# Performance work log

Hardware: AMD Instinct MI355X
Metric: run time of the kernel (lower is better)

Reference implementation:

```python
import jax, jax.numpy as jnp
import numpy as np

B, N, D_OBJ, D_Q, D_FUSED, D_BOX, D_ATT = 64, 36, 2048, 2048, 2048, 4, 512


def setup_inputs() -> dict:
    key = jax.random.key(0)
    ks = jax.random.split(key, 12)
    s = lambda d: 1.0 / np.sqrt(d)
    return {
        "question_embedding": jax.random.normal(ks[0], (B * N, D_Q), jnp.float32),
        "object_features_list": jax.random.normal(ks[1], (B, N, D_OBJ), jnp.float32),
        "bounding_boxes": jax.random.uniform(ks[2], (B, N, D_BOX), jnp.float32),
        "Wq": jax.random.normal(ks[3], (D_Q, D_FUSED), jnp.float32) * s(D_Q),
        "Wo": jax.random.normal(ks[4], (D_OBJ, D_FUSED), jnp.float32) * s(D_OBJ),
        "Wfa": jax.random.normal(ks[5], (D_FUSED, D_FUSED), jnp.float32) * s(D_FUSED),
        "Wfb": jax.random.normal(ks[6], (D_FUSED, D_FUSED), jnp.float32) * s(D_FUSED),
        "Wba": jax.random.normal(ks[7], (D_BOX, D_FUSED), jnp.float32) * s(D_BOX),
        "Wbb": jax.random.normal(ks[8], (D_BOX, D_FUSED), jnp.float32) * s(D_BOX),
        "W0": jax.random.normal(ks[9], (D_FUSED, D_ATT), jnp.float32) * s(D_FUSED),
        "b0": jnp.zeros((D_ATT,), jnp.float32),
        "W1": jax.random.normal(ks[10], (D_ATT, 1), jnp.float32) * s(D_ATT),
        "b1": jnp.zeros((1,), jnp.float32),
        "batch_size": B,
        "num_obj": N,
    }


def reference(question_embedding, object_features_list, bounding_boxes,
              Wq, Wo, Wfa, Wfb, Wba, Wbb, W0, b0, W1, b1,
              batch_size, num_obj):
    # fuse_object_features_with_questions: MLB fusion of question and objects
    obj_flat = object_features_list.reshape(batch_size * num_obj, -1)  # [BN, D]
    fused = (question_embedding @ Wq) * (obj_flat @ Wo)                # [BN, Df]
    fused = fused.reshape(batch_size, num_obj, -1)                     # [B, N, Df]

    # pairwise: project once, broadcast-multiply instead of materializing
    # expanded [B*N*N, D] operands (same math as expand+view+fusion).
    ra = fused @ Wfa                 # [B, N, Df]
    rb = fused @ Wfb                 # [B, N, Df]
    ba = bounding_boxes @ Wba        # [B, N, Df]
    bb = bounding_boxes @ Wbb        # [B, N, Df]
    # relations[b, i, j, :] = fusion_fused(f_i, f_j) + fusion_box(box_i, box_j)
    relations = ra[:, :, None, :] * rb[:, None, :, :] + ba[:, :, None, :] * bb[:, None, :, :]  # [B,N,N,Df]

    # compute_relation_attention: linear-tanh-linear, softmax over dim=2
    h = jnp.tanh(relations @ W0 + b0)          # [B, N, N, D_att]
    scores = h @ W1 + b1                       # [B, N, N, 1]
    att = jax.nn.softmax(scores, axis=2)[..., 0]  # [B, N, N]
    e_hat = jnp.sum(relations * att[..., None], axis=2)  # [B, N, Df]

    pairwise_res = fused + e_hat
    return object_features_list + pairwise_res
```

## Files before the change

kernel.cpp:

```cpp
#include <hip/hip_runtime.h>
#include <hip/hip_bf16.h>
#include <math.h>

constexpr int kB    = 64;
constexpr int kN    = 36;
constexpr int kBN   = kB * kN;
constexpr int kD    = 2048;
constexpr int kDatt = 512;
constexpr int kPairs = kN * kN;

using bf16x8 = __attribute__((ext_vector_type(8))) short;
using f32x4  = __attribute__((ext_vector_type(4))) float;

typedef unsigned int u32;
typedef __attribute__((address_space(3))) u32 lds_u32;
typedef const __attribute__((address_space(1))) u32 glb_u32;

__device__ inline unsigned short f2bf(float f) {
    union { float f; unsigned u; } v; v.f = f;
    unsigned r = v.u + 0x7FFFu + ((v.u >> 16) & 1u);
    return (unsigned short)(r >> 16);
}

__global__ __launch_bounds__(256)
void kcvt(const float* __restrict__ x, unsigned short* __restrict__ y, int n4)
{
    int i = blockIdx.x * 256 + threadIdx.x;
    if (i < n4) {
        float4 v = ((const float4*)x)[i];
        ushort4 o = {f2bf(v.x), f2bf(v.y), f2bf(v.z), f2bf(v.w)};
        ((ushort4*)y)[i] = o;
    }
}

__global__ __launch_bounds__(256)
void ktrp(const float* __restrict__ W, unsigned short* __restrict__ WT, int nt)
{
    __shared__ float T[64][65];
    const int k0 = blockIdx.x * 64;
    const int n0 = blockIdx.y * 64;
    const int c = threadIdx.x & 63, r0 = threadIdx.x >> 6;
    #pragma unroll
    for (int rr = 0; rr < 64; rr += 4)
        T[r0 + rr][c] = W[(size_t)(k0 + r0 + rr) * nt + n0 + c];
    __syncthreads();
    #pragma unroll
    for (int rr = 0; rr < 64; rr += 4)
        WT[(size_t)(n0 + r0 + rr) * kD + k0 + c] = f2bf(T[c][r0 + rr]);
}

__global__ __launch_bounds__(64)
void krepack_w0(const unsigned short* __restrict__ W0T, unsigned short* __restrict__ W0s)
{
    const int kb    = blockIdx.x;
    const int chunk = blockIdx.y;
    const int g     = threadIdx.x;
    const int row = chunk * 16 + (g & 7) + ((g >> 5) << 3);
    const int cg8 = ((g >> 3) & 3) * 8;
    const uint4 v = *(const uint4*)&W0T[(size_t)row * kD + kb * 32 + cg8];
    *(uint4*)&W0s[(size_t)kb * 16384 + chunk * 512 + g * 8] = v;
}

__global__ __launch_bounds__(256)
void k3_box_proj(const float* __restrict__ box, const float* __restrict__ Wba,
                 const float* __restrict__ Wbb,
                 float* __restrict__ ba, float* __restrict__ bb)
{
    const int r = blockIdx.y;
    const int c = blockIdx.x * 256 + threadIdx.x;
    const float x0 = box[r * 4 + 0], x1 = box[r * 4 + 1];
    const float x2 = box[r * 4 + 2], x3 = box[r * 4 + 3];
    float va = x0 * Wba[c] + x1 * Wba[kD + c] + x2 * Wba[2 * kD + c] + x3 * Wba[3 * kD + c];
    float vb = x0 * Wbb[c] + x1 * Wbb[kD + c] + x2 * Wbb[2 * kD + c] + x3 * Wbb[3 * kD + c];
    ba[(size_t)r * kD + c] = va;
    bb[(size_t)r * kD + c] = vb;
}

__device__ inline void stage128(const unsigned short* __restrict__ g,
                                int grow0, int k0,
                                unsigned short* lds, int w, int lane)
{
    const int sr = lane >> 2, sc = (lane & 3) * 8;
    #pragma unroll
    for (int t = 0; t < 2; ++t) {
        int r = w * 32 + t * 16;
        const unsigned short* gp = g + (size_t)(grow0 + r + sr) * kD + k0 + sc;
        __builtin_amdgcn_global_load_lds((glb_u32*)gp, (lds_u32*)(lds + r * 32), 16, 0, 0);
    }
}
__device__ inline void stage64(const unsigned short* __restrict__ g,
                               int grow0, int k0,
                               unsigned short* lds, int w, int lane)
{
    const int sr = lane >> 2, sc = (lane & 3) * 8;
    int r = w * 16;
    const unsigned short* gp = g + (size_t)(grow0 + r + sr) * kD + k0 + sc;
    __builtin_amdgcn_global_load_lds((glb_u32*)gp, (lds_u32*)(lds + r * 32), 16, 0, 0);
}

__global__ __launch_bounds__(256, 2)
void k1_dual_mfma(const unsigned short* __restrict__ Qb,
                  const unsigned short* __restrict__ WqT,
                  const unsigned short* __restrict__ Ob,
                  const unsigned short* __restrict__ WoT,
                  unsigned short* __restrict__ fusedb)
{
    __shared__ __align__(16) unsigned short As1[128][32];
    __shared__ __align__(16) unsigned short As2[128][32];
    __shared__ __align__(16) unsigned short Bs1[64][32];
    __shared__ __align__(16) unsigned short Bs2[64][32];

    const int tid = threadIdx.x;
    const int lane = tid & 63;
    const int w = tid >> 6;
    const int wm = w >> 1, wn = w & 1;
    const int row0 = blockIdx.y * 128;
    const int col0 = blockIdx.x * 64;

    f32x4 acc1[4][2], acc2[4][2];
    #pragma unroll
    for (int mt = 0; mt < 4; ++mt)
        #pragma unroll
        for (int nt = 0; nt < 2; ++nt) { acc1[mt][nt] = (f32x4)(0.f); acc2[mt][nt] = (f32x4)(0.f); }

    const int fr = lane & 15, ko = (lane >> 4) * 8;

    for (int k0 = 0; k0 < kD; k0 += 32) {
        stage128(Qb,  row0, k0, &As1[0][0], w, lane);
        stage128(Ob,  row0, k0, &As2[0][0], w, lane);
        stage64 (WqT, col0, k0, &Bs1[0][0], w, lane);
        stage64 (WoT, col0, k0, &Bs2[0][0], w, lane);
        __syncthreads();

        bf16x8 a1[4], a2[4];
        #pragma unroll
        for (int mt = 0; mt < 4; ++mt) {
            a1[mt] = *(bf16x8*)&As1[wm * 64 + mt * 16 + fr][ko];
            a2[mt] = *(bf16x8*)&As2[wm * 64 + mt * 16 + fr][ko];
        }
        #pragma unroll
        for (int nt = 0; nt < 2; ++nt) {
            bf16x8 b1 = *(bf16x8*)&Bs1[wn * 32 + nt * 16 + fr][ko];
            bf16x8 b2 = *(bf16x8*)&Bs2[wn * 32 + nt * 16 + fr][ko];
            #pragma unroll
            for (int mt = 0; mt < 4; ++mt) {
                acc1[mt][nt] = __builtin_amdgcn_mfma_f32_16x16x32_bf16(a1[mt], b1, acc1[mt][nt], 0, 0, 0);
                acc2[mt][nt] = __builtin_amdgcn_mfma_f32_16x16x32_bf16(a2[mt], b2, acc2[mt][nt], 0, 0, 0);
            }
        }
        __syncthreads();
    }

    const int fq = lane >> 4;
    #pragma unroll
    for (int mt = 0; mt < 4; ++mt)
        #pragma unroll
        for (int nt = 0; nt < 2; ++nt) {
            int row = row0 + wm * 64 + mt * 16 + fq * 4;
            int col = col0 + wn * 32 + nt * 16 + fr;
            #pragma unroll
            for (int reg = 0; reg < 4; ++reg) {
                float v = acc1[mt][nt][reg] * acc2[mt][nt][reg];
                fusedb[(size_t)(row + reg) * kD + col] = f2bf(v);
            }
        }
}

__global__ __launch_bounds__(256, 2)
void k2_dual_mfma(const unsigned short* __restrict__ Fb,
                  const unsigned short* __restrict__ WfaT,
                  const unsigned short* __restrict__ WfbT,
                  float* __restrict__ ra, float* __restrict__ rb)
{
    __shared__ __align__(16) unsigned short As [128][32];
    __shared__ __align__(16) unsigned short Bs1[64][32];
    __shared__ __align__(16) unsigned short Bs2[64][32];

    const int tid = threadIdx.x;
    const int lane = tid & 63;
    const int w = tid >> 6;
    const int wm = w >> 1, wn = w & 1;
    const int row0 = blockIdx.y * 128;
    const int col0 = blockIdx.x * 64;

    f32x4 acc1[4][2], acc2[4][2];
    #pragma unroll
    for (int mt = 0; mt < 4; ++mt)
        #pragma unroll
        for (int nt = 0; nt < 2; ++nt) { acc1[mt][nt] = (f32x4)(0.f); acc2[mt][nt] = (f32x4)(0.f); }

    const int fr = lane & 15, ko = (lane >> 4) * 8;

    for (int k0 = 0; k0 < kD; k0 += 32) {
        stage128(Fb,   row0, k0, &As [0][0], w, lane);
        stage64 (WfaT, col0, k0, &Bs1[0][0], w, lane);
        stage64 (WfbT, col0, k0, &Bs2[0][0], w, lane);
        __syncthreads();

        bf16x8 a[4];
        #pragma unroll
        for (int mt = 0; mt < 4; ++mt)
            a[mt] = *(bf16x8*)&As[wm * 64 + mt * 16 + fr][ko];
        #pragma unroll
        for (int nt = 0; nt < 2; ++nt) {
            bf16x8 b1 = *(bf16x8*)&Bs1[wn * 32 + nt * 16 + fr][ko];
            bf16x8 b2 = *(bf16x8*)&Bs2[wn * 32 + nt * 16 + fr][ko];
            #pragma unroll
            for (int mt = 0; mt < 4; ++mt) {
                acc1[mt][nt] = __builtin_amdgcn_mfma_f32_16x16x32_bf16(a[mt], b1, acc1[mt][nt], 0, 0, 0);
                acc2[mt][nt] = __builtin_amdgcn_mfma_f32_16x16x32_bf16(a[mt], b2, acc2[mt][nt], 0, 0, 0);
            }
        }
        __syncthreads();
    }

    const int fq = lane >> 4;
    #pragma unroll
    for (int mt = 0; mt < 4; ++mt)
        #pragma unroll
        for (int nt = 0; nt < 2; ++nt) {
            int row = row0 + wm * 64 + mt * 16 + fq * 4;
            int col = col0 + wn * 32 + nt * 16 + fr;
            #pragma unroll
            for (int reg = 0; reg < 4; ++reg) {
                size_t o = (size_t)(row + reg) * kD + col;
                ra[o] = acc1[mt][nt][reg];
                rb[o] = acc2[mt][nt][reg];
            }
        }
}

__global__ __launch_bounds__(1024)
void k4_scores_mfma(const float* __restrict__ ra, const float* __restrict__ rb,
                    const float* __restrict__ ba, const float* __restrict__ bb,
                    const unsigned short* __restrict__ W0s,
                    const float* __restrict__ b0, const float* __restrict__ W1,
                    float* __restrict__ scores)
{
    __shared__ __align__(16) unsigned short Bs[2][512 * 32];
    __shared__ __align__(16) unsigned short RelS[2][128][40];
    __shared__ __align__(16) float4 Stg4[2][714];
    __shared__ float scoreS[128];

    const int tid  = threadIdx.x;
    const int lane = tid & 63;
    const int w    = tid >> 6;
    const int wm   = w >> 3;
    const int wn   = w & 7;

    const int work = (blockIdx.x & 7) * 88 + (blockIdx.x >> 3);
    const int b    = work / 11;
    const int tile = work - b * 11;
    const int p0   = tile * 128;
    const int i0   = p0 / kN;

    const float* raB = ra + (size_t)b * kN * kD;
    const float* rbB = rb + (size_t)b * kN * kD;
    const float* baB = ba + (size_t)b * kN * kD;
    const float* bbB = bb + (size_t)b * kN * kD;

    const bool hasStage = (tid < 672);
    const float* sptr;
    int sdst;
    {
        int s = hasStage ? tid : 671;
        int row = s >> 4, t4 = s & 15;
        int arr = t4 >> 3, q = t4 & 7;
        int grow; const float* base;
        if (row < 6) {
            int il = (row < 5) ? row : 4;
            grow = i0 + il; if (grow > kN - 1) grow = kN - 1;
            base = arr ? baB : raB;
        } else {
            grow = row - 6;
            base = arr ? bbB : rbB;
        }
        sptr = base + (size_t)grow * kD + q * 4;
        sdst = row * 17 + t4;
    }

    int rowA, cgA, ilA, jA;
    {
        rowA = tid >> 3; cgA = tid & 7;
        int p = p0 + rowA; if (p >= kPairs) p = kPairs - 1;
        int i = p / kN;
        jA  = p - i * kN;
        ilA = i - i0;
    }

    const int fr = lane & 15, fq = lane >> 4;
    const int bco = ((fr & 7) << 3) + ((fr >> 3) << 8) + (fq << 6);

    f32x4 acc[4][4];
    #pragma unroll
    for (int mt = 0; mt < 4; ++mt)
        #pragma unroll
        for (int nt = 0; nt < 4; ++nt)
            acc[mt][nt] = (f32x4)(0.f);

    if (tid < 128) scoreS[tid] = 0.f;

    float4 sreg0;

    #define ISSUE_B(k0_, buf_)                                                   \
        _Pragma("unroll")                                                        \
        for (int t = 0; t < 2; ++t) {                                            \
            int chunk = w * 2 + t;                                               \
            const unsigned short* gp = W0s + (size_t)((k0_) >> 5) * 16384        \
                                       + chunk * 512 + lane * 8;                 \
            __builtin_amdgcn_global_load_lds((glb_u32*)gp,                       \
                (lds_u32*)&Bs[buf_][chunk * 512], 16, 0, 0);                     \
        }

    #define STAGE_LOAD(k0_) {                                                    \
            if (hasStage) sreg0 = *(const float4*)(sptr + (k0_));                \
        }

    #define STAGE_WRITE(buf_) {                                                  \
            if (hasStage) Stg4[buf_][sdst] = sreg0;                              \
        }

    #define REL_GEN(buf_) {                                                      \
            float4 va = Stg4[buf_][ilA * 17 + cgA];                              \
            float4 vb = Stg4[buf_][ilA * 17 + 8 + cgA];                          \
            float4 vr = Stg4[buf_][(6 + jA) * 17 + cgA];                         \
            float4 vq = Stg4[buf_][(6 + jA) * 17 + 8 + cgA];                     \
            ushort4 o;                                                           \
            o.x = f2bf(va.x * vr.x + vb.x * vq.x);                               \
            o.y = f2bf(va.y * vr.y + vb.y * vq.y);                               \
            o.z = f2bf(va.z * vr.z + vb.z * vq.z);                               \
            o.w = f2bf(va.w * vr.w + vb.w * vq.w);                               \
            *(ushort4*)&RelS[buf_][rowA][cgA * 4] = o;                           \
        }

    STAGE_LOAD(0)
    STAGE_WRITE(0)
    STAGE_LOAD(32)
    __syncthreads();
    REL_GEN(0)
    STAGE_WRITE(1)
    ISSUE_B(0, 0)

    for (int k = 0; k < 64; ++k) {
        const int cur = k & 1, nxt = cur ^ 1;
        __syncthreads();
        if (k < 62) STAGE_LOAD((k + 2) * 32)
        if (k < 63) ISSUE_B((k + 1) * 32, nxt)
        bf16x8 af[4];
        #pragma unroll
        for (int mt = 0; mt < 4; ++mt)
            af[mt] = *(bf16x8*)&RelS[cur][wm * 64 + mt * 16 + fr][fq * 8];
        #pragma unroll
        for (int nt = 0; nt < 4; ++nt) {
            bf16x8 bfv = *(bf16x8*)&Bs[cur][wn * 2048 + nt * 512 + bco];
            #pragma unroll
            for (int mt = 0; mt < 4; ++mt)
                acc[mt][nt] = __builtin_amdgcn_mfma_f32_16x16x32_bf16(af[mt], bfv, acc[mt][nt], 0, 0, 0);
        }
        if (k < 62) STAGE_WRITE(cur)
        if (k < 63) REL_GEN(nxt)
    }

    float b0v[4], w1v[4];
    #pragma unroll
    for (int nt = 0; nt < 4; ++nt) {
        int col = wn * 64 + nt * 16 + fr;
        b0v[nt] = b0[col];
        w1v[nt] = W1[col];
    }
    #pragma unroll
    for (int mt = 0; mt < 4; ++mt) {
        #pragma unroll
        for (int reg = 0; reg < 4; ++reg) {
            float p = 0.f;
            #pragma unroll
            for (int nt = 0; nt < 4; ++nt)
                p += w1v[nt] * tanhf(acc[mt][nt][reg] + b0v[nt]);
            p += __shfl_xor(p, 1, 64);
            p += __shfl_xor(p, 2, 64);
            p += __shfl_xor(p, 4, 64);
            p += __shfl_xor(p, 8, 64);
            if (fr == 0)
                atomicAdd(&scoreS[wm * 64 + mt * 16 + fq * 4 + reg], p);
        }
    }
    __syncthreads();
    if (tid < 128 && p0 + tid < kPairs)
        scores[(size_t)b * kPairs + p0 + tid] = scoreS[tid];
}

__global__ __launch_bounds__(64)
void k5_softmax(const float* __restrict__ scores, float* __restrict__ att)
{
    const int bi = blockIdx.x;
    const int tid = threadIdx.x;
    float s = (tid < kN) ? scores[(size_t)bi * kN + tid] : -1e30f;
    float m = s;
    #pragma unroll
    for (int off = 32; off >= 1; off >>= 1)
        m = fmaxf(m, __shfl_xor(m, off, 64));
    float e = (tid < kN) ? expf(s - m) : 0.f;
    float sum = e;
    #pragma unroll
    for (int off = 32; off >= 1; off >>= 1)
        sum += __shfl_xor(sum, off, 64);
    if (tid < kN) att[(size_t)bi * kN + tid] = e / sum;
}

__global__ __launch_bounds__(256)
void k6_output(const float* __restrict__ obj, const unsigned short* __restrict__ fusedb,
               const float* __restrict__ ra, const float* __restrict__ ba,
               const float* __restrict__ rb, const float* __restrict__ bb,
               const float* __restrict__ att, float* __restrict__ out)
{
    __shared__ float attS[kN];
    const int bi = blockIdx.x;
    const int b = bi / kN;
    const int tid = threadIdx.x;
    if (tid < kN) attS[tid] = att[(size_t)bi * kN + tid];
    __syncthreads();
    for (int d = tid; d < kD; d += 256) {
        float s1 = 0.f, s2 = 0.f;
        #pragma unroll 4
        for (int j = 0; j < kN; ++j) {
            float a = attS[j];
            size_t rrow = (size_t)(b * kN + j) * kD + d;
            s1 = fmaf(a, rb[rrow], s1);
            s2 = fmaf(a, bb[rrow], s2);
        }
        size_t o = (size_t)bi * kD + d;
        float fv = __uint_as_float((u32)fusedb[o] << 16);
        out[o] = obj[o] + fv + ra[o] * s1 + ba[o] * s2;
    }
}

extern "C" void kernel_launch(void* const* d_in, const int* in_sizes, int n_in,
                              void* d_out, int out_size, void* d_ws, size_t ws_size,
                              hipStream_t stream)
{
    const float* q   = (const float*)d_in[0];
    const float* obj = (const float*)d_in[1];
    const float* box = (const float*)d_in[2];
    const float* Wq  = (const float*)d_in[3];
    const float* Wo  = (const float*)d_in[4];
    const float* Wfa = (const float*)d_in[5];
    const float* Wfb = (const float*)d_in[6];
    const float* Wba = (const float*)d_in[7];
    const float* Wbb = (const float*)d_in[8];
    const float* W0  = (const float*)d_in[9];
    const float* b0v = (const float*)d_in[10];
    const float* W1  = (const float*)d_in[11];
    float* out = (float*)d_out;

    const size_t nBD = (size_t)kBN * kD;
    float* ws = (float*)d_ws;
    size_t off = 0;
    float* ra     = ws + off; off += nBD;
    float* rb     = ws + off; off += nBD;
    float* ba     = ws + off; off += nBD;
    float* bb     = ws + off; off += nBD;
    float* scores = ws + off; off += (size_t)kBN * kN;
    float* att    = ws + off; off += (size_t)kBN * kN;

    unsigned short* us = (unsigned short*)(ws + off);
    size_t uoff = 0;
    unsigned short* W0T     = us + uoff; uoff += (size_t)kDatt * kD;
    unsigned short* W0s     = us + uoff; uoff += (size_t)kDatt * kD;
    unsigned short* q_bf    = us + uoff; uoff += nBD;
    unsigned short* obj_bf  = us + uoff; uoff += nBD;
    unsigned short* fusedbf = us + uoff; uoff += nBD;
    unsigned short* WqT     = us + uoff; uoff += (size_t)kD * kD;
    unsigned short* WoT     = us + uoff; uoff += (size_t)kD * kD;
    unsigned short* WfaT = q_bf;
    unsigned short* WfbT = obj_bf;

    const int n4 = (int)(nBD / 4);
    kcvt<<<dim3((n4 + 255) / 256), 256, 0, stream>>>(q,   q_bf,   n4);
    kcvt<<<dim3((n4 + 255) / 256), 256, 0, stream>>>(obj, obj_bf, n4);
    ktrp<<<dim3(32, 32), 256, 0, stream>>>(Wq, WqT, kD);
    ktrp<<<dim3(32, 32), 256, 0, stream>>>(Wo, WoT, kD);
    ktrp<<<dim3(32, 8),  256, 0, stream>>>(W0, W0T, kDatt);
    krepack_w0<<<dim3(kD / 32, kDatt / 16), 64, 0, stream>>>(W0T, W0s);
    k3_box_proj<<<dim3(kD / 256, kBN), 256, 0, stream>>>(box, Wba, Wbb, ba, bb);

    k1_dual_mfma<<<dim3(kD / 64, kBN / 128), 256, 0, stream>>>(q_bf, WqT, obj_bf, WoT, fusedbf);

    ktrp<<<dim3(32, 32), 256, 0, stream>>>(Wfa, WfaT, kD);
    ktrp<<<dim3(32, 32), 256, 0, stream>>>(Wfb, WfbT, kD);

    k2_dual_mfma<<<dim3(kD / 64, kBN / 128), 256, 0, stream>>>(fusedbf, WfaT, WfbT, ra, rb);

    k4_scores_mfma<<<dim3(kB * 11), 1024, 0, stream>>>(ra, rb, ba, bb, W0s, b0v, W1, scores);
    k5_softmax<<<kBN, 64, 0, stream>>>(scores, att);
    k6_output<<<kBN, 256, 0, stream>>>(obj, fusedbf, ra, ba, rb, bb, att, out);
}
```

Baseline: 666.4 us.

## Fold box relation term into precomputed W0 projection as extra K step

```diff
diff --git a/kernel.cpp b/kernel.cpp
--- a/kernel.cpp
+++ b/kernel.cpp
@@ -59,6 +59,39 @@
     const int cg8 = ((g >> 3) & 3) * 8;
     const uint4 v = *(const uint4*)&W0T[(size_t)row * kD + kb * 32 + cg8];
     *(uint4*)&W0s[(size_t)kb * 16384 + chunk * 512 + g * 8] = v;
+}
+
+__global__ __launch_bounds__(128)
+void kgbox(const float* __restrict__ Wba, const float* __restrict__ Wbb,
+           const float* __restrict__ W0, float* __restrict__ G)
+{
+    const int uv = blockIdx.x;
+    const int u = uv >> 2, v = uv & 3;
+    const int c = blockIdx.y * 128 + threadIdx.x;
+    float acc = 0.f;
+    for (int k = 0; k < kD; k += 4) {
+        #pragma unroll
+        for (int t = 0; t < 4; ++t)
+            acc = fmaf(Wba[u * kD + k + t] * Wbb[v * kD + k + t],
+                       W0[(size_t)(k + t) * kDatt + c], acc);
+    }
+    G[(size_t)uv * kDatt + c] = acc;
+}
+
+__global__ __launch_bounds__(64)
+void krepack_g(const float* __restrict__ G, unsigned short* __restrict__ W0s)
+{
+    const int chunk = blockIdx.x;
+    const int g     = threadIdx.x;
+    const int col = chunk * 16 + (g & 7) + ((g >> 5) << 3);
+    const int kg  = (g >> 3) & 3;
+    unsigned short o[8];
+    #pragma unroll
+    for (int e = 0; e < 8; ++e) {
+        int kl = kg * 8 + e;
+        o[e] = (kl < 16) ? f2bf(G[(size_t)kl * kDatt + col]) : (unsigned short)0;
+    }
+    *(uint4*)&W0s[(size_t)64 * 16384 + chunk * 512 + g * 8] = *(uint4*)o;
 }
 
 __global__ __launch_bounds__(256)
@@ -232,14 +265,14 @@
 
 __global__ __launch_bounds__(1024)
 void k4_scores_mfma(const float* __restrict__ ra, const float* __restrict__ rb,
-                    const float* __restrict__ ba, const float* __restrict__ bb,
+                    const float* __restrict__ box,
                     const unsigned short* __restrict__ W0s,
                     const float* __restrict__ b0, const float* __restrict__ W1,
                     float* __restrict__ scores)
 {
     __shared__ __align__(16) unsigned short Bs[2][512 * 32];
     __shared__ __align__(16) unsigned short RelS[2][128][40];
-    __shared__ __align__(16) float4 Stg4[2][714];
+    __shared__ __align__(16) float4 Stg4[2][378];
     __shared__ float scoreS[128];
 
     const int tid  = threadIdx.x;
@@ -254,38 +287,36 @@
     const int p0   = tile * 128;
     const int i0   = p0 / kN;
 
-    const float* raB = ra + (size_t)b * kN * kD;
-    const float* rbB = rb + (size_t)b * kN * kD;
-    const float* baB = ba + (size_t)b * kN * kD;
-    const float* bbB = bb + (size_t)b * kN * kD;
-
-    const bool hasStage = (tid < 672);
+    const float* raB  = ra  + (size_t)b * kN * kD;
+    const float* rbB  = rb  + (size_t)b * kN * kD;
+    const float* boxB = box + (size_t)b * kN * 4;
+
+    const bool hasStage = (tid < 336);
     const float* sptr;
     int sdst;
     {
-        int s = hasStage ? tid : 671;
-        int row = s >> 4, t4 = s & 15;
-        int arr = t4 >> 3, q = t4 & 7;
+        int s = hasStage ? tid : 335;
+        int row = s >> 3, q = s & 7;
         int grow; const float* base;
         if (row < 6) {
             int il = (row < 5) ? row : 4;
             grow = i0 + il; if (grow > kN - 1) grow = kN - 1;
-            base = arr ? baB : raB;
+            base = raB;
         } else {
             grow = row - 6;
-            base = arr ? bbB : rbB;
+            base = rbB;
         }
         sptr = base + (size_t)grow * kD + q * 4;
-        sdst = row * 17 + t4;
-    }
-
-    int rowA, cgA, ilA, jA;
+        sdst = row * 9 + q;
+    }
+
+    int rowA, cgA, ilA, iA, jA;
     {
         rowA = tid >> 3; cgA = tid & 7;
         int p = p0 + rowA; if (p >= kPairs) p = kPairs - 1;
-        int i = p / kN;
-        jA  = p - i * kN;
-        ilA = i - i0;
+        iA  = p / kN;
+        jA  = p - iA * kN;
+        ilA = iA - i0;
     }
 
     const int fr = lane & 15, fq = lane >> 4;
@@ -321,15 +352,28 @@
         }
 
     #define REL_GEN(buf_) {                                                      \
-            float4 va = Stg4[buf_][ilA * 17 + cgA];                              \
-            float4 vb = Stg4[buf_][ilA * 17 + 8 + cgA];                          \
-            float4 vr = Stg4[buf_][(6 + jA) * 17 + cgA];                         \
-            float4 vq = Stg4[buf_][(6 + jA) * 17 + 8 + cgA];                     \
+            float4 va = Stg4[buf_][ilA * 9 + cgA];                               \
+            float4 vr = Stg4[buf_][(6 + jA) * 9 + cgA];                          \
             ushort4 o;                                                           \
-            o.x = f2bf(va.x * vr.x + vb.x * vq.x);                               \
-            o.y = f2bf(va.y * vr.y + vb.y * vq.y);                               \
-            o.z = f2bf(va.z * vr.z + vb.z * vq.z);                               \
-            o.w = f2bf(va.w * vr.w + vb.w * vq.w);                               \
+            o.x = f2bf(va.x * vr.x);                                             \
+            o.y = f2bf(va.y * vr.y);                                             \
+            o.z = f2bf(va.z * vr.z);                                             \
+            o.w = f2bf(va.w * vr.w);                                             \
+            *(ushort4*)&RelS[buf_][rowA][cgA * 4] = o;                           \
+        }
+
+    #define REL_GEN_BOX(buf_) {                                                  \
+            ushort4 o = {0, 0, 0, 0};                                            \
+            if (cgA < 4) {                                                       \
+                float4 bi = *(const float4*)(boxB + iA * 4);                     \
+                float4 bj = *(const float4*)(boxB + jA * 4);                     \
+                float biu = (cgA == 0) ? bi.x : (cgA == 1) ? bi.y                \
+                          : (cgA == 2) ? bi.z : bi.w;                            \
+                o.x = f2bf(biu * bj.x);                                          \
+                o.y = f2bf(biu * bj.y);                                          \
+                o.z = f2bf(biu * bj.z);                                          \
+                o.w = f2bf(biu * bj.w);                                          \
+            }                                                                    \
             *(ushort4*)&RelS[buf_][rowA][cgA * 4] = o;                           \
         }
 
@@ -341,11 +385,11 @@
     STAGE_WRITE(1)
     ISSUE_B(0, 0)
 
-    for (int k = 0; k < 64; ++k) {
+    for (int k = 0; k <= 64; ++k) {
         const int cur = k & 1, nxt = cur ^ 1;
         __syncthreads();
         if (k < 62) STAGE_LOAD((k + 2) * 32)
-        if (k < 63) ISSUE_B((k + 1) * 32, nxt)
+        if (k < 64) ISSUE_B((k + 1) * 32, nxt)
         bf16x8 af[4];
         #pragma unroll
         for (int mt = 0; mt < 4; ++mt)
@@ -359,6 +403,7 @@
         }
         if (k < 62) STAGE_WRITE(cur)
         if (k < 63) REL_GEN(nxt)
+        else if (k == 63) REL_GEN_BOX(nxt)
     }
 
     float b0v[4], w1v[4];
@@ -461,11 +506,12 @@
     float* bb     = ws + off; off += nBD;
     float* scores = ws + off; off += (size_t)kBN * kN;
     float* att    = ws + off; off += (size_t)kBN * kN;
+    float* G      = ws + off; off += (size_t)16 * kDatt;
 
     unsigned short* us = (unsigned short*)(ws + off);
     size_t uoff = 0;
     unsigned short* W0T     = us + uoff; uoff += (size_t)kDatt * kD;
-    unsigned short* W0s     = us + uoff; uoff += (size_t)kDatt * kD;
+    unsigned short* W0s     = us + uoff; uoff += (size_t)65 * 16384;
     unsigned short* q_bf    = us + uoff; uoff += nBD;
     unsigned short* obj_bf  = us + uoff; uoff += nBD;
     unsigned short* fusedbf = us + uoff; uoff += nBD;
@@ -481,6 +527,8 @@
     ktrp<<<dim3(32, 32), 256, 0, stream>>>(Wo, WoT, kD);
     ktrp<<<dim3(32, 8),  256, 0, stream>>>(W0, W0T, kDatt);
     krepack_w0<<<dim3(kD / 32, kDatt / 16), 64, 0, stream>>>(W0T, W0s);
+    kgbox<<<dim3(16, 4), 128, 0, stream>>>(Wba, Wbb, W0, G);
+    krepack_g<<<dim3(32), 64, 0, stream>>>(G, W0s);
     k3_box_proj<<<dim3(kD / 256, kBN), 256, 0, stream>>>(box, Wba, Wbb, ba, bb);
 
     k1_dual_mfma<<<dim3(kD / 64, kBN / 128), 256, 0, stream>>>(q_bf, WqT, obj_bf, WoT, fusedbf);
@@ -490,7 +538,7 @@
 
     k2_dual_mfma<<<dim3(kD / 64, kBN / 128), 256, 0, stream>>>(fusedbf, WfaT, WfbT, ra, rb);
 
-    k4_scores_mfma<<<dim3(kB * 11), 1024, 0, stream>>>(ra, rb, ba, bb, W0s, b0v, W1, scores);
+    k4_scores_mfma<<<dim3(kB * 11), 1024, 0, stream>>>(ra, rb, box, W0s, b0v, W1, scores);
     k5_softmax<<<kBN, 64, 0, stream>>>(scores, att);
     k6_output<<<kBN, 256, 0, stream>>>(obj, fusedbf, ra, ba, rb, bb, att, out);
 }
```

Measured after the change: 760.9 us. 14.2% more time.
